# Performance work log

Measured on AMD Instinct MI355X. Metric: run time of the kernel, lower is better.

## Reference

```python
import jax, jax.numpy as jnp
import numpy as np

N, D = 8192, 256
NUM_CLASSES = 128
MARGIN = 0.2


def setup_inputs() -> dict:
    key = jax.random.key(0)
    k1, k2 = jax.random.split(key)
    embeddings = jax.random.normal(k1, (N, D), dtype=jnp.float32)
    labels = jax.random.randint(k2, (N,), 0, NUM_CLASSES, dtype=jnp.int64)
    return {"embeddings": embeddings, "labels": labels}


def reference(embeddings, labels):
    n = embeddings.shape[0]
    # cosine distance matrix: 1 - cos_sim, clipped to [0, 2]
    norm = jnp.sqrt(jnp.sum(embeddings * embeddings, axis=-1, keepdims=True))
    normed = embeddings / jnp.maximum(norm, 1e-12)
    sim = normed @ normed.T                      # (N, N)
    dist = jnp.clip(1.0 - sim, 0.0, 2.0)

    same = labels[:, None] == labels[None, :]    # (N, N) same-class mask
    eye = jnp.eye(n, dtype=bool)
    cand = same & ~eye                           # valid positives per anchor
    valid = cand.any(axis=1)                     # anchors with >=1 positive
    pos_idx = jnp.argmax(cand, axis=1)           # first same-class index != i

    rows = jnp.arange(n)
    d_ap = dist[rows, pos_idx]                   # (N,)

    # semi-hard mining: negatives with d_ap < d < d_ap + margin, fallback hardest
    neg = ~same                                  # different class (self excluded)
    semi = neg & (dist > d_ap[:, None]) & (dist < d_ap[:, None] + MARGIN)
    has_semi = semi.any(axis=1)
    inf = jnp.asarray(jnp.inf, dist.dtype)
    d_semi = jnp.where(semi, dist, inf)
    d_hard = jnp.where(neg, dist, inf)
    neg_idx = jnp.where(has_semi, jnp.argmin(d_semi, axis=1), jnp.argmin(d_hard, axis=1))

    d_an = dist[rows, neg_idx]
    losses = jnp.maximum(d_ap - d_an + MARGIN, 0.0) * valid.astype(dist.dtype)
    cnt = valid.sum().astype(dist.dtype)
    return jnp.where(cnt > 0, losses.sum() / cnt, jnp.zeros((), dist.dtype))
```

## Files before the change

### kernel.cpp

```cpp
#include <hip/hip_runtime.h>
#include <math.h>

#define NN 8192
#define DD 256
#define MARGIN 0.2f
#define SL 16
#define CPS (NN / SL)
#define TILES (CPS / 64)
#define IMAX 0x7fffffff

typedef __attribute__((ext_vector_type(4))) float f32x4;
typedef __attribute__((ext_vector_type(2))) long long2_t;
typedef __attribute__((ext_vector_type(8))) int i32x8;
typedef unsigned int u32;
typedef unsigned char u8;

static __device__ __forceinline__ u8 f2e4m3(float x) {
    float a = fabsf(x);
    a = fminf(a, 448.0f);
    const u32 s = (__float_as_uint(x) >> 31) << 7;
    if (a < 0.015625f) {
        const int m = (int)rintf(a * 512.0f);
        return (u8)(s | m);
    }
    u32 u = __float_as_uint(a);
    u += 0x7FFFF + ((u >> 20) & 1);
    const u32 e = (u >> 23) - 120;
    return (u8)(s | (e << 3) | ((u >> 20) & 7));
}

static __device__ __forceinline__ i32x8 pack8(long2_t lo, long2_t hi) {
    union { long2_t l2[2]; i32x8 v; } u;
    u.l2[0] = lo; u.l2[1] = hi;
    return u.v;
}

#define GLOAD16(g, l)                                                             \
    __builtin_amdgcn_global_load_lds(                                             \
        (const __attribute__((address_space(1))) void*)(g),                       \
        (__attribute__((address_space(3))) void*)(l), 16, 0, 0)

static __device__ __forceinline__ void comb2(int& a1, int& a2, int b1, int b2) {
    const int lo = min(a1, b1);
    const int hi = max(a1, b1);
    a2 = min(hi, min(a2, b2));
    a1 = lo;
}

__global__ void kprepclass(const float* __restrict__ emb, const int* __restrict__ labels,
                           u8* __restrict__ E8, float* __restrict__ invn,
                           int* __restrict__ posidx, u32* __restrict__ cnt_done) {
    const int tid = threadIdx.x;
    if (blockIdx.x < 2048) {
        const int wid = tid >> 6, l = tid & 63;
        const int row = blockIdx.x * 4 + wid;
        const float4 v = *(const float4*)&emb[(size_t)row * DD + l * 4];
        float ss = v.x * v.x + v.y * v.y + v.z * v.z + v.w * v.w;
#pragma unroll
        for (int o = 1; o < 64; o <<= 1) ss += __shfl_xor(ss, o);
        const float inv = 1.0f / fmaxf(sqrtf(ss), 1e-12f);
        if (l == 0) invn[row] = inv;
        const u32 b0 = f2e4m3(v.x * inv), b1 = f2e4m3(v.y * inv);
        const u32 b2 = f2e4m3(v.z * inv), b3 = f2e4m3(v.w * inv);
        const u32 packed = b0 | (b1 << 8) | (b2 << 16) | (b3 << 24);
        *(u32*)&E8[(size_t)row * DD + l * 4] = packed;
    } else {
        const int c = blockIdx.x - 2048;
        if (c == 0 && tid == 0) *cnt_done = 0;
        int m1 = IMAX, m2 = IMAX;
        for (int j = tid; j < NN; j += 256) {
            if (labels[j] == c) {
                if (m1 == IMAX) m1 = j;
                else if (m2 == IMAX) m2 = j;
            }
        }
#pragma unroll
        for (int o = 1; o < 64; o <<= 1)
            comb2(m1, m2, __shfl_xor(m1, o), __shfl_xor(m2, o));
        __shared__ int s1[4], s2[4];
        __shared__ int bj1, bj2;
        const int wave = tid >> 6, lane = tid & 63;
        if (lane == 0) { s1[wave] = m1; s2[wave] = m2; }
        __syncthreads();
        if (tid == 0) {
            comb2(m1, m2, s1[1], s2[1]);
            comb2(m1, m2, s1[2], s2[2]);
            comb2(m1, m2, s1[3], s2[3]);
            bj1 = m1; bj2 = m2;
        }
        __syncthreads();
        const int j1 = bj1, j2 = bj2;
        for (int j = tid; j < NN; j += 256)
            if (labels[j] == c) posidx[j] = (j2 == IMAX) ? -1 : ((j == j1) ? j2 : j1);
    }
}

__global__ void kdap(const float* __restrict__ emb, const float* __restrict__ invn,
                     const int* __restrict__ posidx, float* __restrict__ dap) {
    const int wid = threadIdx.x >> 6, l = threadIdx.x & 63;
    const int i = blockIdx.x * 4 + wid;
    const int p = posidx[i];
    float dv = 0.0f;
    if (p >= 0) {
        const float4 a = *(const float4*)&emb[(size_t)i * DD + l * 4];
        const float4 b = *(const float4*)&emb[(size_t)p * DD + l * 4];
        float s = a.x * b.x + a.y * b.y + a.z * b.z + a.w * b.w;
#pragma unroll
        for (int o = 1; o < 64; o <<= 1) s += __shfl_xor(s, o);
        const float sim = s * invn[i] * invn[p];
        dv = fminf(fmaxf(1.0f - sim, 0.0f), 2.0f);
    }
    if (l == 0) dap[i] = dv;
}

__global__ __launch_bounds__(256, 3) void kmine(
    const u8* __restrict__ E8, const int* __restrict__ labels,
    const float* __restrict__ dap, float* __restrict__ pM1, float* __restrict__ pMN)
{
    __shared__ __align__(16) u8 At0[64 * 256], At1[64 * 256];
    __shared__ __align__(16) int Ls[CPS];
    __shared__ float RedN[2][128], RedS[2][128];

    const int tid = threadIdx.x;
    const int l = tid & 63;
    const int wid = tid >> 6;
    const int wr = wid >> 1;
    const int wc = wid & 1;
    const int slice = blockIdx.x;
    const int a0 = blockIdx.y * 128;

    const int frow = l & 15;
    const int fq = l >> 4;

    if (tid < 128) {
        const int4 lv = *(const int4*)&labels[slice * CPS + tid * 4];
        *(int4*)&Ls[tid * 4] = lv;
    }
    int la[4]; float hiv[4];
#pragma unroll
    for (int n = 0; n < 4; ++n) {
        const int ai = a0 + wc * 64 + n * 16 + frow;
        la[n] = labels[ai];
        hiv[n] = 1.0f - dap[ai];
    }
    const char* Ec = (const char*)E8;
    i32x8 breg[4][2];
#pragma unroll
    for (int n = 0; n < 4; ++n)
#pragma unroll
        for (int kh = 0; kh < 2; ++kh) {
            const char* p = Ec + (size_t)(a0 + wc * 64 + n * 16 + frow) * 256
                               + kh * 128 + fq * 32;
            breg[n][kh] = pack8(*(const long2_t*)p, *(const long2_t*)(p + 16));
        }

    const char* asrc = Ec + ((size_t)(slice * CPS) + (tid >> 4)) * 256
                          + (((tid & 15) ^ (tid >> 4)) * 16);

#define STAGE(BUF, OFF) do {                                    \
        _Pragma("unroll")                                       \
        for (int i = 0; i < 4; ++i)                             \
            GLOAD16(asrc + (OFF) + i * 4096,                    \
                    &BUF[tid * 16 + i * 4096]);                 \
    } while (0)

    float mN[4], m1[4];
#pragma unroll
    for (int n = 0; n < 4; ++n) { mN[n] = -INFINITY; m1[n] = -INFINITY; }
    const f32x4 Zv = {0.f, 0.f, 0.f, 0.f};
    f32x4 acc[2][4];

#define COMPTILE(BUF, T) do {                                                       \
        _Pragma("unroll")                                                           \
        for (int kh = 0; kh < 2; ++kh) {                                            \
            i32x8 a8[2];                                                            \
            _Pragma("unroll")                                                       \
            for (int m = 0; m < 2; ++m) {                                           \
                const int row = wr * 32 + m * 16 + frow;                            \
                const int cb = kh * 8 + fq * 2;                                     \
                const int p0 = (cb ^ (row & 15)) * 16;                              \
                const int p1 = ((cb + 1) ^ (row & 15)) * 16;                        \
                a8[m] = pack8(*(const long2_t*)&BUF[row * 256 + p0],                \
                              *(const long2_t*)&BUF[row * 256 + p1]);               \
            }                                                                       \
            __builtin_amdgcn_s_setprio(1);                                          \
            _Pragma("unroll")                                                       \
            for (int m = 0; m < 2; ++m)                                             \
                _Pragma("unroll")                                                   \
                for (int n = 0; n < 4; ++n)                                         \
                    acc[m][n] = __builtin_amdgcn_mfma_scale_f32_16x16x128_f8f6f4(   \
                        a8[m], breg[n][kh], (kh == 0) ? Zv : acc[m][n],             \
                        0, 0, 0, 0x7F7F7F7F, 0, 0x7F7F7F7F);                        \
            __builtin_amdgcn_s_setprio(0);                                          \
        }                                                                           \
        {                                                                           \
            int lcv[8];                                                             \
            _Pragma("unroll")                                                       \
            for (int m = 0; m < 2; ++m) {                                           \
                const int4 v = *(const int4*)&Ls[(T) * 64 + wr * 32 + m * 16        \
                                                 + fq * 4];                        \
                lcv[m * 4 + 0] = v.x; lcv[m * 4 + 1] = v.y;                         \
                lcv[m * 4 + 2] = v.z; lcv[m * 4 + 3] = v.w;                         \
            }                                                                       \
            _Pragma("unroll")                                                       \
            for (int n = 0; n < 4; ++n) {                                           \
                _Pragma("unroll")                                                   \
                for (int m = 0; m < 2; ++m)                                         \
                    _Pragma("unroll")                                               \
                    for (int r = 0; r < 4; ++r) {                                   \
                        const float sv = acc[m][n][r];                              \
                        const float sel = (lcv[m * 4 + r] != la[n]) ? sv            \
                                                                    : -INFINITY;    \
                        mN[n] = fmaxf(mN[n], sel);                                  \
                        m1[n] = fmaxf(m1[n], (sel < hiv[n]) ? sel : -INFINITY);     \
                    }                                                               \
            }                                                                       \
        }                                                                           \
    } while (0)

    STAGE(At0, 0);
    asm volatile("s_waitcnt lgkmcnt(0)" ::: "memory");

#pragma unroll
    for (int t = 0; t < TILES; ++t) {
        if (t + 1 < TILES) {
            if (t & 1) STAGE(At0, (t + 1) * 16384);
            else       STAGE(At1, (t + 1) * 16384);
        }
        if (t + 1 < TILES)
            asm volatile("s_waitcnt vmcnt(4)" ::: "memory");
        else
            asm volatile("s_waitcnt vmcnt(0)" ::: "memory");
        __builtin_amdgcn_s_barrier();
        if (t & 1) COMPTILE(At1, t);
        else       COMPTILE(At0, t);
        __builtin_amdgcn_s_barrier();
    }
#undef STAGE
#undef COMPTILE

#pragma unroll
    for (int n = 0; n < 4; ++n) {
        mN[n] = fmaxf(mN[n], __shfl_xor(mN[n], 16));
        mN[n] = fmaxf(mN[n], __shfl_xor(mN[n], 32));
        m1[n] = fmaxf(m1[n], __shfl_xor(m1[n], 16));
        m1[n] = fmaxf(m1[n], __shfl_xor(m1[n], 32));
    }
    __syncthreads();
    if (fq == 0) {
#pragma unroll
        for (int n = 0; n < 4; ++n) {
            if (wr == 0) {
                RedN[0][wc * 64 + n * 16 + frow] = mN[n];
                RedS[0][wc * 64 + n * 16 + frow] = m1[n];
            } else {
                RedN[1][wc * 64 + n * 16 + frow] = mN[n];
                RedS[1][wc * 64 + n * 16 + frow] = m1[n];
            }
        }
    }
    __syncthreads();
    if (tid < 128) {
        pMN[slice * NN + a0 + tid] = fmaxf(RedN[0][tid], RedN[1][tid]);
        pM1[slice * NN + a0 + tid] = fmaxf(RedS[0][tid], RedS[1][tid]);
    }
}

__global__ void kcombine(const int* __restrict__ posidx, const float* __restrict__ dap,
                         const float* __restrict__ pM1, const float* __restrict__ pMN,
                         float* __restrict__ partials, u32* __restrict__ cnt_done,
                         float* __restrict__ out)
{
    const int i = blockIdx.x * 256 + threadIdx.x;
    float loss = 0.0f, cnt = 0.0f;
    if (posidx[i] >= 0) {
        float s1 = -INFINITY, sN = -INFINITY;
#pragma unroll
        for (int s = 0; s < SL; ++s) {
            s1 = fmaxf(s1, pM1[s * NN + i]);
            sN = fmaxf(sN, pMN[s * NN + i]);
        }
        const float da = dap[i];
        const float lo = 1.0f - da - MARGIN;
        const float M = (s1 > lo) ? s1 : sN;
        const float dan = fminf(fmaxf(1.0f - M, 0.0f), 2.0f);
        loss = fmaxf(da - dan + MARGIN, 0.0f);
        cnt = 1.0f;
    }
#pragma unroll
    for (int off = 1; off < 64; off <<= 1) {
        loss += __shfl_xor(loss, off);
        cnt  += __shfl_xor(cnt, off);
    }
    __shared__ float sl[4], sc[4];
    __shared__ int last;
    const int wave = threadIdx.x >> 6, lane = threadIdx.x & 63;
    if (lane == 0) { sl[wave] = loss; sc[wave] = cnt; }
    __syncthreads();
    if (threadIdx.x == 0) {
        partials[blockIdx.x]      = sl[0] + sl[1] + sl[2] + sl[3];
        partials[32 + blockIdx.x] = sc[0] + sc[1] + sc[2] + sc[3];
        __threadfence();
        last = (atomicAdd(cnt_done, 1u) == 31u);
    }
    __syncthreads();
    if (last && threadIdx.x < 64) {
        const int t = threadIdx.x;
        float L = (t < 32) ? partials[t] : 0.0f;
        float C = (t < 32) ? partials[32 + t] : 0.0f;
#pragma unroll
        for (int off = 1; off < 64; off <<= 1) {
            L += __shfl_xor(L, off);
            C += __shfl_xor(C, off);
        }
        if (t == 0) out[0] = (C > 0.0f) ? (L / C) : 0.0f;
    }
}

extern "C" void kernel_launch(void* const* d_in, const int* in_sizes, int n_in,
                              void* d_out, int out_size, void* d_ws, size_t ws_size,
                              hipStream_t stream) {
    const float* emb  = (const float*)d_in[0];
    const int* labels = (const int*)d_in[1];
    float* out = (float*)d_out;

    char* w = (char*)d_ws;
    u8*    E8   = (u8*)w;                        w += (size_t)NN * DD;
    float* invn = (float*)w;                     w += NN * 4;
    float* dapv = (float*)w;                     w += NN * 4;
    int*   posi = (int*)w;                       w += NN * 4;
    float* pM1  = (float*)w;                     w += (size_t)SL * NN * 4;
    float* pMN  = (float*)w;                     w += (size_t)SL * NN * 4;
    float* parts = (float*)w;                    w += 64 * 4;
    u32*   cdone = (u32*)w;

    kprepclass<<<2048 + 128, 256, 0, stream>>>(emb, labels, E8, invn, posi, cdone);
    kdap<<<NN / 4, 256, 0, stream>>>(emb, invn, posi, dapv);
    kmine<<<dim3(SL, NN / 128), 256, 0, stream>>>(E8, labels, dapv, pM1, pMN);
    kcombine<<<NN / 256, 256, 0, stream>>>(posi, dapv, pM1, pMN, parts, cdone, out);
}
```

Baseline: 52.53 us.

## Give each wave private LDS double buffers and drop per-tile block barriers

Each wave now stages only the 32 candidate rows it consumes into its own double-buffered LDS region, so the per-tile workgroup barriers can be removed and waves proceed independently, synchronised only by vmcnt waits. This duplicates the A-tile loads across the two waves sharing a row group, doubling global/LDS staging traffic, and enlarges LDS from 32KB to 64KB per block. The launch_bounds occupancy hint of 3 is also dropped, which may reduce occupancy given the larger LDS footprint.

```diff
diff --git a/kernel.cpp b/kernel.cpp
--- a/kernel.cpp
+++ b/kernel.cpp
@@ -113,11 +113,11 @@
     if (l == 0) dap[i] = dv;
 }
 
-__global__ __launch_bounds__(256, 3) void kmine(
+__global__ __launch_bounds__(256) void kmine(
     const u8* __restrict__ E8, const int* __restrict__ labels,
     const float* __restrict__ dap, float* __restrict__ pM1, float* __restrict__ pMN)
 {
-    __shared__ __align__(16) u8 At0[64 * 256], At1[64 * 256];
+    __shared__ __align__(16) u8 Ab[4][2][32 * 256];
     __shared__ __align__(16) int Ls[CPS];
     __shared__ float RedN[2][128], RedS[2][128];
 
@@ -128,12 +128,13 @@
     const int wc = wid & 1;
     const int slice = blockIdx.x;
     const int a0 = blockIdx.y * 128;
+    const int c0 = slice * CPS;
 
     const int frow = l & 15;
     const int fq = l >> 4;
 
     if (tid < 128) {
-        const int4 lv = *(const int4*)&labels[slice * CPS + tid * 4];
+        const int4 lv = *(const int4*)&labels[c0 + tid * 4];
         *(int4*)&Ls[tid * 4] = lv;
     }
     int la[4]; float hiv[4];
@@ -154,14 +155,23 @@
             breg[n][kh] = pack8(*(const long2_t*)p, *(const long2_t*)(p + 16));
         }
 
-    const char* asrc = Ec + ((size_t)(slice * CPS) + (tid >> 4)) * 256
-                          + (((tid & 15) ^ (tid >> 4)) * 16);
-
-#define STAGE(BUF, OFF) do {                                    \
-        _Pragma("unroll")                                       \
-        for (int i = 0; i < 4; ++i)                             \
-            GLOAD16(asrc + (OFF) + i * 4096,                    \
-                    &BUF[tid * 16 + i * 4096]);                 \
+    const int rl = l >> 4;
+    const int cp = l & 15;
+    int soff[4];
+#pragma unroll
+    for (int j = 0; j < 4; ++j) {
+        const int r = rl + 4 * j;
+        soff[j] = r * 256 + ((cp ^ (r & 15)) * 16);
+    }
+    const char* wbase = Ec + (size_t)(c0 + wr * 32) * 256;
+    u8* buf0 = &Ab[wid][0][0];
+    u8* buf1 = &Ab[wid][1][0];
+
+#define STAGE(BUF, TOFF) do {                                        \
+        _Pragma("unroll")                                            \
+        for (int i = 0; i < 8; ++i)                                  \
+            GLOAD16(wbase + (TOFF) + soff[i & 3] + (i >> 2) * 4096,  \
+                    (BUF) + i * 1024 + l * 16);                      \
     } while (0)
 
     float mN[4], m1[4];
@@ -176,12 +186,12 @@
             i32x8 a8[2];                                                            \
             _Pragma("unroll")                                                       \
             for (int m = 0; m < 2; ++m) {                                           \
-                const int row = wr * 32 + m * 16 + frow;                            \
+                const int lr = m * 16 + frow;                                       \
                 const int cb = kh * 8 + fq * 2;                                     \
-                const int p0 = (cb ^ (row & 15)) * 16;                              \
-                const int p1 = ((cb + 1) ^ (row & 15)) * 16;                        \
-                a8[m] = pack8(*(const long2_t*)&BUF[row * 256 + p0],                \
-                              *(const long2_t*)&BUF[row * 256 + p1]);               \
+                const int p0 = (cb ^ frow) * 16;                                    \
+                const int p1 = ((cb + 1) ^ frow) * 16;                              \
+                a8[m] = pack8(*(const long2_t*)&(BUF)[lr * 256 + p0],               \
+                              *(const long2_t*)&(BUF)[lr * 256 + p1]);              \
             }                                                                       \
             __builtin_amdgcn_s_setprio(1);                                          \
             _Pragma("unroll")                                                       \
@@ -218,23 +228,21 @@
         }                                                                           \
     } while (0)
 
-    STAGE(At0, 0);
+    STAGE(buf0, 0);
     asm volatile("s_waitcnt lgkmcnt(0)" ::: "memory");
+    __builtin_amdgcn_s_barrier();
 
 #pragma unroll
     for (int t = 0; t < TILES; ++t) {
         if (t + 1 < TILES) {
-            if (t & 1) STAGE(At0, (t + 1) * 16384);
-            else       STAGE(At1, (t + 1) * 16384);
-        }
-        if (t + 1 < TILES)
-            asm volatile("s_waitcnt vmcnt(4)" ::: "memory");
-        else
+            if (t & 1) STAGE(buf0, (t + 1) * 16384);
+            else       STAGE(buf1, (t + 1) * 16384);
+            asm volatile("s_waitcnt vmcnt(8)" ::: "memory");
+        } else {
             asm volatile("s_waitcnt vmcnt(0)" ::: "memory");
-        __builtin_amdgcn_s_barrier();
-        if (t & 1) COMPTILE(At1, t);
-        else       COMPTILE(At0, t);
-        __builtin_amdgcn_s_barrier();
+        }
+        if (t & 1) COMPTILE(buf1, t);
+        else       COMPTILE(buf0, t);
     }
 #undef STAGE
 #undef COMPTILE
```

Measured after the change: 56.86 us. 8.2% more time.

## Exploit symmetry of similarity matrix by computing only upper-triangular tile pairs

Applied to the files above, without the earlier changes.

The mining kernel now launches a 64x64 grid of 128x128 panel pairs and skips those below the diagonal, so each off-diagonal tile's similarities are reduced both along rows (for the anchor panel) and along columns (for the other panel). Column-wise max reductions use per-tile shuffles and shared-memory buffers. Partial results grow from 16 slices to 64 panels per anchor, so the combine kernel reads four times more partial data. This roughly halves the MFMA work, at the cost of extra reduction shuffles, a larger grid with many early-exit blocks, and more partial-result traffic.

```diff
diff --git a/kernel.cpp b/kernel.cpp
--- a/kernel.cpp
+++ b/kernel.cpp
@@ -4,9 +4,7 @@
 #define NN 8192
 #define DD 256
 #define MARGIN 0.2f
-#define SL 16
-#define CPS (NN / SL)
-#define TILES (CPS / 64)
+#define NPAN 64
 #define IMAX 0x7fffffff
 
 typedef __attribute__((ext_vector_type(4))) float f32x4;
@@ -113,27 +111,32 @@
     if (l == 0) dap[i] = dv;
 }
 
-__global__ __launch_bounds__(256, 3) void kmine(
+__global__ __launch_bounds__(256) void kmine(
     const u8* __restrict__ E8, const int* __restrict__ labels,
     const float* __restrict__ dap, float* __restrict__ pM1, float* __restrict__ pMN)
 {
+    const int cpan = blockIdx.x;
+    const int rpan = blockIdx.y;
+    if (rpan > cpan) return;
+
     __shared__ __align__(16) u8 At0[64 * 256], At1[64 * 256];
-    __shared__ __align__(16) int Ls[CPS];
+    __shared__ __align__(16) int Ls[128];
     __shared__ float RedN[2][128], RedS[2][128];
+    __shared__ float RedCN[2][128], RedCS[2][128];
 
     const int tid = threadIdx.x;
     const int l = tid & 63;
     const int wid = tid >> 6;
     const int wr = wid >> 1;
     const int wc = wid & 1;
-    const int slice = blockIdx.x;
-    const int a0 = blockIdx.y * 128;
+    const int a0 = cpan * 128;
+    const int c0 = rpan * 128;
 
     const int frow = l & 15;
     const int fq = l >> 4;
 
-    if (tid < 128) {
-        const int4 lv = *(const int4*)&labels[slice * CPS + tid * 4];
+    if (tid < 32) {
+        const int4 lv = *(const int4*)&labels[c0 + tid * 4];
         *(int4*)&Ls[tid * 4] = lv;
     }
     int la[4]; float hiv[4];
@@ -143,6 +146,15 @@
         la[n] = labels[ai];
         hiv[n] = 1.0f - dap[ai];
     }
+    float hivc[2][8];
+#pragma unroll
+    for (int T = 0; T < 2; ++T)
+#pragma unroll
+        for (int m = 0; m < 2; ++m) {
+            const float4 hv = *(const float4*)&dap[c0 + T * 64 + wr * 32 + m * 16 + fq * 4];
+            hivc[T][m * 4 + 0] = 1.0f - hv.x; hivc[T][m * 4 + 1] = 1.0f - hv.y;
+            hivc[T][m * 4 + 2] = 1.0f - hv.z; hivc[T][m * 4 + 3] = 1.0f - hv.w;
+        }
     const char* Ec = (const char*)E8;
     i32x8 breg[4][2];
 #pragma unroll
@@ -154,7 +166,7 @@
             breg[n][kh] = pack8(*(const long2_t*)p, *(const long2_t*)(p + 16));
         }
 
-    const char* asrc = Ec + ((size_t)(slice * CPS) + (tid >> 4)) * 256
+    const char* asrc = Ec + ((size_t)c0 + (tid >> 4)) * 256
                           + (((tid & 15) ^ (tid >> 4)) * 16);
 
 #define STAGE(BUF, OFF) do {                                    \
@@ -202,6 +214,9 @@
                 lcv[m * 4 + 0] = v.x; lcv[m * 4 + 1] = v.y;                         \
                 lcv[m * 4 + 2] = v.z; lcv[m * 4 + 3] = v.w;                         \
             }                                                                       \
+            float mNc[8], m1c[8];                                                   \
+            _Pragma("unroll")                                                       \
+            for (int i = 0; i < 8; ++i) { mNc[i] = -INFINITY; m1c[i] = -INFINITY; } \
             _Pragma("unroll")                                                       \
             for (int n = 0; n < 4; ++n) {                                           \
                 _Pragma("unroll")                                                   \
@@ -213,6 +228,27 @@
                                                                     : -INFINITY;    \
                         mN[n] = fmaxf(mN[n], sel);                                  \
                         m1[n] = fmaxf(m1[n], (sel < hiv[n]) ? sel : -INFINITY);     \
+                        mNc[m * 4 + r] = fmaxf(mNc[m * 4 + r], sel);                \
+                        m1c[m * 4 + r] = fmaxf(m1c[m * 4 + r],                      \
+                            (sel < hivc[T][m * 4 + r]) ? sel : -INFINITY);          \
+                    }                                                               \
+            }                                                                       \
+            _Pragma("unroll")                                                       \
+            for (int i = 0; i < 8; ++i) {                                           \
+                _Pragma("unroll")                                                   \
+                for (int o = 1; o < 16; o <<= 1) {                                  \
+                    mNc[i] = fmaxf(mNc[i], __shfl_xor(mNc[i], o));                  \
+                    m1c[i] = fmaxf(m1c[i], __shfl_xor(m1c[i], o));                  \
+                }                                                                   \
+            }                                                                       \
+            if (frow == 0) {                                                        \
+                _Pragma("unroll")                                                   \
+                for (int m = 0; m < 2; ++m)                                         \
+                    _Pragma("unroll")                                               \
+                    for (int r = 0; r < 4; ++r) {                                   \
+                        const int idx = (T) * 64 + wr * 32 + m * 16 + fq * 4 + r;   \
+                        RedCN[wc][idx] = mNc[m * 4 + r];                            \
+                        RedCS[wc][idx] = m1c[m * 4 + r];                            \
                     }                                                               \
             }                                                                       \
         }                                                                           \
@@ -221,21 +257,14 @@
     STAGE(At0, 0);
     asm volatile("s_waitcnt lgkmcnt(0)" ::: "memory");
 
-#pragma unroll
-    for (int t = 0; t < TILES; ++t) {
-        if (t + 1 < TILES) {
-            if (t & 1) STAGE(At0, (t + 1) * 16384);
-            else       STAGE(At1, (t + 1) * 16384);
-        }
-        if (t + 1 < TILES)
-            asm volatile("s_waitcnt vmcnt(4)" ::: "memory");
-        else
-            asm volatile("s_waitcnt vmcnt(0)" ::: "memory");
-        __builtin_amdgcn_s_barrier();
-        if (t & 1) COMPTILE(At1, t);
-        else       COMPTILE(At0, t);
-        __builtin_amdgcn_s_barrier();
-    }
+    STAGE(At1, 16384);
+    asm volatile("s_waitcnt vmcnt(4)" ::: "memory");
+    __builtin_amdgcn_s_barrier();
+    COMPTILE(At0, 0);
+    __builtin_amdgcn_s_barrier();
+    asm volatile("s_waitcnt vmcnt(0)" ::: "memory");
+    __builtin_amdgcn_s_barrier();
+    COMPTILE(At1, 1);
 #undef STAGE
 #undef COMPTILE
 
@@ -250,19 +279,25 @@
     if (fq == 0) {
 #pragma unroll
         for (int n = 0; n < 4; ++n) {
-            if (wr == 0) {
-                RedN[0][wc * 64 + n * 16 + frow] = mN[n];
-                RedS[0][wc * 64 + n * 16 + frow] = m1[n];
-            } else {
-                RedN[1][wc * 64 + n * 16 + frow] = mN[n];
-                RedS[1][wc * 64 + n * 16 + frow] = m1[n];
-            }
+            RedN[wr][wc * 64 + n * 16 + frow] = mN[n];
+            RedS[wr][wc * 64 + n * 16 + frow] = m1[n];
         }
     }
     __syncthreads();
     if (tid < 128) {
-        pMN[slice * NN + a0 + tid] = fmaxf(RedN[0][tid], RedN[1][tid]);
-        pM1[slice * NN + a0 + tid] = fmaxf(RedS[0][tid], RedS[1][tid]);
+        const float aN = fmaxf(RedN[0][tid], RedN[1][tid]);
+        const float aS = fmaxf(RedS[0][tid], RedS[1][tid]);
+        const float cN = fmaxf(RedCN[0][tid], RedCN[1][tid]);
+        const float cS = fmaxf(RedCS[0][tid], RedCS[1][tid]);
+        if (rpan == cpan) {
+            pMN[(size_t)rpan * NN + a0 + tid] = fmaxf(aN, cN);
+            pM1[(size_t)rpan * NN + a0 + tid] = fmaxf(aS, cS);
+        } else {
+            pMN[(size_t)rpan * NN + a0 + tid] = aN;
+            pM1[(size_t)rpan * NN + a0 + tid] = aS;
+            pMN[(size_t)cpan * NN + c0 + tid] = cN;
+            pM1[(size_t)cpan * NN + c0 + tid] = cS;
+        }
     }
 }
 
@@ -275,10 +310,10 @@
     float loss = 0.0f, cnt = 0.0f;
     if (posidx[i] >= 0) {
         float s1 = -INFINITY, sN = -INFINITY;
-#pragma unroll
-        for (int s = 0; s < SL; ++s) {
-            s1 = fmaxf(s1, pM1[s * NN + i]);
-            sN = fmaxf(sN, pMN[s * NN + i]);
+#pragma unroll 8
+        for (int s = 0; s < NPAN; ++s) {
+            s1 = fmaxf(s1, pM1[(size_t)s * NN + i]);
+            sN = fmaxf(sN, pMN[(size_t)s * NN + i]);
         }
         const float da = dap[i];
         const float lo = 1.0f - da - MARGIN;
@@ -329,13 +364,13 @@
     float* invn = (float*)w;                     w += NN * 4;
     float* dapv = (float*)w;                     w += NN * 4;
     int*   posi = (int*)w;                       w += NN * 4;
-    float* pM1  = (float*)w;                     w += (size_t)SL * NN * 4;
-    float* pMN  = (float*)w;                     w += (size_t)SL * NN * 4;
+    float* pM1  = (float*)w;                     w += (size_t)NPAN * NN * 4;
+    float* pMN  = (float*)w;                     w += (size_t)NPAN * NN * 4;
     float* parts = (float*)w;                    w += 64 * 4;
     u32*   cdone = (u32*)w;
 
     kprepclass<<<2048 + 128, 256, 0, stream>>>(emb, labels, E8, invn, posi, cdone);
     kdap<<<NN / 4, 256, 0, stream>>>(emb, invn, posi, dapv);
-    kmine<<<dim3(SL, NN / 128), 256, 0, stream>>>(E8, labels, dapv, pM1, pMN);
+    kmine<<<dim3(NPAN, NPAN), 256, 0, stream>>>(E8, labels, dapv, pM1, pMN);
     kcombine<<<NN / 256, 256, 0, stream>>>(posi, dapv, pM1, pMN, parts, cdone, out);
 }
```

Result: slower. 82.71 us (+57.4%).
